# Performance work log

Hardware: AMD Instinct MI355X
Metric: run time of the kernel (lower is better)

Reference implementation:

```python
import jax, jax.numpy as jnp
import numpy as np

D_MODEL = 1024
D_INNER = 2048
D_STATE = 16
D_CONV = 4
DT_RANK = 64  # ceil(D_MODEL / 16)
BATCH = 2
SEQLEN = 2048


def setup_inputs() -> dict:
    key = jax.random.key(0)
    ks = jax.random.split(key, 9)
    s = 0.02
    hidden_states = jax.random.normal(ks[0], (BATCH, SEQLEN, D_MODEL), dtype=jnp.float32)
    W_in = jax.random.normal(ks[1], (D_MODEL, 2 * D_INNER), dtype=jnp.float32) * s
    # flax depthwise Conv kernel layout: (window, in_features//groups=1, out_features)
    conv_kernel = jax.random.normal(ks[2], (D_CONV, 1, D_INNER), dtype=jnp.float32) * 0.2
    conv_bias = jax.random.normal(ks[3], (D_INNER,), dtype=jnp.float32) * s
    W_x = jax.random.normal(ks[4], (D_INNER, DT_RANK + 2 * D_STATE), dtype=jnp.float32) * s
    W_dt = jax.random.normal(ks[5], (DT_RANK, D_INNER), dtype=jnp.float32) * s
    b_dt = jax.random.normal(ks[6], (D_INNER,), dtype=jnp.float32) * s
    # A_log = log(arange(1, d_state+1)) broadcast over d_inner (constant init in module)
    A_log = jnp.log(jnp.broadcast_to(jnp.arange(1, D_STATE + 1, dtype=jnp.float32), (D_INNER, D_STATE)))
    D = jnp.ones((D_INNER,), dtype=jnp.float32)
    W_out = jax.random.normal(ks[7], (D_INNER, D_MODEL), dtype=jnp.float32) * s
    return {
        "hidden_states": hidden_states,
        "W_in": W_in,
        "conv_kernel": conv_kernel,
        "conv_bias": conv_bias,
        "W_x": W_x,
        "W_dt": W_dt,
        "b_dt": b_dt,
        "A_log": A_log,
        "D": D,
        "W_out": W_out,
    }


def _mamba_forward(hidden_states, W_in, conv_kernel, conv_bias, W_x, W_dt, b_dt, A_log, D, W_out):
    # in_proj, then einops '(d i)' split with i=2 => interleaved channels
    xz = hidden_states @ W_in                       # (b, l, 2*d_inner)
    x = xz[..., 0::2]                               # (b, l, d_inner)
    z = xz[..., 1::2]                               # (b, l, d_inner)

    # depthwise conv1d, padding='SAME' (as in flax nn.Conv)
    x = jax.lax.conv_general_dilated(
        x, conv_kernel, window_strides=(1,), padding="SAME",
        dimension_numbers=("NWC", "WIO", "NWC"),
        feature_group_count=D_INNER,
    ) + conv_bias
    x = jax.nn.silu(x)

    x_dbl = x @ W_x                                 # (b, l, dt_rank + 2*d_state)
    dt = x_dbl[..., :DT_RANK] @ W_dt + b_dt         # (b, l, d_inner)
    Bm = x_dbl[..., DT_RANK:DT_RANK + D_STATE]      # (b, l, n)
    Cm = x_dbl[..., DT_RANK + D_STATE:]             # (b, l, n)

    A = -jnp.exp(A_log.astype(jnp.float32))         # (d_inner, n)
    delta = jax.nn.softplus(dt.astype(jnp.float32)) # (b, l, d_inner)

    deltaA = jnp.exp(jnp.einsum("bld,dn->lbdn", delta, A))          # (l, b, d, n)
    deltaB_u = jnp.einsum("bld,bln,bld->lbdn", delta, Bm, x)        # (l, b, d, n)
    C_l = jnp.transpose(Cm, (1, 0, 2))                               # (l, b, n)

    state0 = jnp.zeros((BATCH, D_INNER, D_STATE), dtype=jnp.float32)

    def step(state, inputs):
        dA, dBu, c = inputs
        state = dA * state + dBu                    # (b, d, n)
        y = jnp.einsum("bdn,bn->bd", state, c)      # (b, d)
        return state, y

    _, y = jax.lax.scan(step, state0, (deltaA, deltaB_u, C_l))
    y = jnp.transpose(y, (1, 0, 2))                 # (b, l, d_inner)

    out = (y + x * D) * jax.nn.silu(z)              # skip via D, gate via silu(z)
    return out @ W_out                              # (b, l, d_model)


def reference(hidden_states, W_in, conv_kernel, conv_bias, W_x, W_dt, b_dt, A_log, D, W_out):
    return _mamba_forward(hidden_states, W_in, conv_kernel, conv_bias, W_x, W_dt, b_dt, A_log, D, W_out)
```

## Files before the change

### kernel.cpp

```cpp
#include <hip/hip_runtime.h>
#include <hip/hip_bf16.h>

typedef unsigned short u16;
typedef __attribute__((ext_vector_type(8))) short short8;
typedef __attribute__((ext_vector_type(4))) short short4v;
typedef __attribute__((ext_vector_type(4))) float f32x4;
typedef __attribute__((ext_vector_type(4))) float float4v;
typedef __attribute__((ext_vector_type(2))) float f32x2;

#define DMODEL 1024
#define DI 2048
#define NST 16
#define RANK 64
#define BB 2
#define LL 2048
#define MM (BB*LL)
#define LC 32
#define NCH (LL/LC)

__device__ __forceinline__ float b2f(u16 v){ union{unsigned u; float f;}x; x.u=(unsigned)v<<16; return x.f; }
__device__ __forceinline__ u16 f2b(float f){
  union{unsigned u; float f;}x; x.f=f;
  unsigned r = x.u + 0x7FFFu + ((x.u>>16)&1u);
  return (u16)(r>>16);
}
__device__ __forceinline__ bool probe_bf(const u16* probe){ return probe[1] != 0; }
__device__ __forceinline__ float ldin(const void* p, size_t i, bool bf){
  return bf ? b2f(((const u16*)p)[i]) : ((const float*)p)[i];
}
__device__ __forceinline__ u16 ldb(const void* p, size_t i, bool bf){
  return bf ? ((const u16*)p)[i] : f2b(((const float*)p)[i]);
}
__device__ __forceinline__ void gl16(const u16* g, char* lds_wave_base){
  __builtin_amdgcn_global_load_lds((const __attribute__((address_space(1))) unsigned*)g,
                                   (__attribute__((address_space(3))) unsigned*)lds_wave_base, 16, 0, 0);
}

template<int EPI>
__global__ __launch_bounds__(512,2) void mgemm256_k(
    const u16* __restrict__ A, const u16* __restrict__ Bt,
    void* __restrict__ O0, void* __restrict__ O1,
    int M, int N, int K, int lda, int ldb, int ldc)
{
  __shared__ char smem[131072];
  const int t = threadIdx.x;
  int bx = blockIdx.x, by = blockIdx.y;
  {
    const int gx = gridDim.x;
    const int nwg = gx*gridDim.y;
    const int lin = by*gx + bx;
    const int swz = (lin & 7)*(nwg>>3) + (lin>>3);
    bx = swz % gx; by = swz / gx;
  }
  const int m0 = by*256, n0 = bx*256;
  const int kbeg = blockIdx.z * K;
  const int wv = t >> 6, ln = t & 63;
  const int wr = wv >> 2, wc = wv & 3;
  const int lr = ln & 15, q = ln >> 4;
  const int NT = K >> 6;

  const int srow = ln >> 3;
  const int koff = ((ln & 7) ^ srow) * 8;
  const u16* AgP[4]; const u16* BgP[4];
#pragma unroll
  for(int c=0;c<4;c++){
    AgP[c] = A + (size_t)(m0 + (c*8+wv)*8 + srow)*lda + kbeg + koff;
    BgP[c] = Bt + (size_t)(n0 + (c*8+wv)*8 + srow)*ldb + kbeg + koff;
  }

  const int ck = ((q ^ (ln & 7)) * 16);
  int aro[8], bro[4];
#pragma unroll
  for(int i=0;i<8;i++) aro[i] = (wr*128 + i*16 + lr)*128 + ck;
#pragma unroll
  for(int j=0;j<4;j++) bro[j] = (wc*64 + j*16 + lr)*128 + ck;

  f32x4 acc[8][4];
#pragma unroll
  for(int i=0;i<8;i++)
#pragma unroll
    for(int j=0;j<4;j++) acc[i][j] = (f32x4){0.f,0.f,0.f,0.f};

  auto stage = [&](int kt, int cur){
    char* ab = smem + cur*65536;
    char* bb = ab + 32768;
#pragma unroll
    for(int c=0;c<4;c++) gl16(AgP[c] + kt*64, ab + (c*8+wv)*1024);
#pragma unroll
    for(int c=0;c<4;c++) gl16(BgP[c] + kt*64, bb + (c*8+wv)*1024);
  };

  stage(0,0);
  stage(1,1);

  for(int kt=0; kt<NT; ++kt){
    const int cur = kt & 1;
    if(kt == NT-1) asm volatile("s_waitcnt vmcnt(0)" ::: "memory");
    else           asm volatile("s_waitcnt vmcnt(8)" ::: "memory");
    __builtin_amdgcn_sched_barrier(0);
    __builtin_amdgcn_s_barrier();
    __builtin_amdgcn_sched_barrier(0);
    const char* ab = smem + cur*65536;
    const char* bb = ab + 32768;
    short8 afr[4], bfr[4];
#pragma unroll
    for(int j=0;j<4;j++) bfr[j] = *(const short8*)(bb + bro[j]);
#pragma unroll
    for(int i=0;i<4;i++) afr[i] = *(const short8*)(ab + aro[i]);
    __builtin_amdgcn_s_setprio(1);
#pragma unroll
    for(int i=0;i<4;i++)
#pragma unroll
      for(int j=0;j<4;j++)
        acc[i][j] = __builtin_amdgcn_mfma_f32_16x16x32_bf16(afr[i], bfr[j], acc[i][j], 0,0,0);
    __builtin_amdgcn_s_setprio(0);
#pragma unroll
    for(int i=0;i<4;i++) afr[i] = *(const short8*)(ab + aro[4+i]);
    __builtin_amdgcn_s_setprio(1);
#pragma unroll
    for(int i=0;i<4;i++)
#pragma unroll
      for(int j=0;j<4;j++)
        acc[4+i][j] = __builtin_amdgcn_mfma_f32_16x16x32_bf16(afr[i], bfr[j], acc[4+i][j], 0,0,0);
    __builtin_amdgcn_s_setprio(0);
#pragma unroll
    for(int j=0;j<4;j++) bfr[j] = *(const short8*)(bb + (bro[j]^64));
#pragma unroll
    for(int i=0;i<4;i++) afr[i] = *(const short8*)(ab + (aro[i]^64));
    __builtin_amdgcn_s_setprio(1);
#pragma unroll
    for(int i=0;i<4;i++)
#pragma unroll
      for(int j=0;j<4;j++)
        acc[i][j] = __builtin_amdgcn_mfma_f32_16x16x32_bf16(afr[i], bfr[j], acc[i][j], 0,0,0);
    __builtin_amdgcn_s_setprio(0);
#pragma unroll
    for(int i=0;i<4;i++) afr[i] = *(const short8*)(ab + (aro[4+i]^64));
    asm volatile("s_waitcnt lgkmcnt(0)" ::: "memory");
    __builtin_amdgcn_sched_barrier(0);
    __builtin_amdgcn_s_barrier();
    __builtin_amdgcn_sched_barrier(0);
    if(kt+2 < NT) stage(kt+2, cur);
    __builtin_amdgcn_sched_barrier(0);
    __builtin_amdgcn_s_setprio(1);
#pragma unroll
    for(int i=0;i<4;i++)
#pragma unroll
      for(int j=0;j<4;j++)
        acc[4+i][j] = __builtin_amdgcn_mfma_f32_16x16x32_bf16(afr[i], bfr[j], acc[4+i][j], 0,0,0);
    __builtin_amdgcn_s_setprio(0);
  }

  if(EPI==4){
    u16* tile = (u16*)smem;
    u16* obase = (n0 < DI) ? (u16*)O0 : (u16*)O1;
    const int cb = n0 & (DI-1);
    for(int h=0;h<2;h++){
      __builtin_amdgcn_s_barrier();
      if(wr == h){
#pragma unroll
        for(int i=0;i<8;i++)
#pragma unroll
          for(int r=0;r<4;r++){
            int trow = i*16 + q*4 + r;
#pragma unroll
            for(int j=0;j<4;j++)
              tile[trow*264 + wc*64 + j*16 + lr] = f2b(acc[i][j][r]);
          }
      }
      asm volatile("s_waitcnt lgkmcnt(0)" ::: "memory");
      __builtin_amdgcn_sched_barrier(0);
      __builtin_amdgcn_s_barrier();
      __builtin_amdgcn_sched_barrier(0);
#pragma unroll
      for(int it=0;it<8;it++){
        int idx = it*512 + t;
        int row = idx >> 5;
        int ch  = (idx & 31) * 8;
        short8 v = *(const short8*)(tile + row*264 + ch);
        *(short8*)(obase + (size_t)(m0 + h*128 + row)*ldc + cb + ch) = v;
      }
    }
    return;
  }
#pragma unroll
  for(int i=0;i<8;i++){
#pragma unroll
    for(int r=0;r<4;r++){
      int row = m0 + wr*128 + i*16 + q*4 + r;
#pragma unroll
      for(int j=0;j<4;j++){
        int col = n0 + wc*64 + j*16 + lr;
        ((float*)O0)[(size_t)blockIdx.z*M*ldc + (size_t)row*ldc + col] = acc[i][j][r];
      }
    }
  }
}

template<int EPI>
__global__ __launch_bounds__(256,2) void mgemm_k(
    const u16* __restrict__ A, const u16* __restrict__ Bt,
    void* __restrict__ O0, void* __restrict__ O1,
    const void* __restrict__ bias, const u16* __restrict__ probe,
    int M, int N, int K, int lda, int ldb, int ldc)
{
  const bool bf = probe_bf(probe);
  __shared__ char smem[(EPI==3) ? 33792 : 16384];
  const int t = threadIdx.x;
  int bx = blockIdx.x, by = blockIdx.y;
  {
    const int gx = gridDim.x;
    const int nwg = gx*gridDim.y;
    const int lin = by*gx + bx;
    const int swz = (lin & 7)*(nwg>>3) + (lin>>3);
    bx = swz % gx; by = swz / gx;
  }
  const int m0 = by*128, n0 = bx*128;
  const int kbeg = blockIdx.z * K;
  const int lane = t & 63;
  const int wv = t >> 6;
  const int wm = (wv>>1)*64, wn = (wv&1)*64;
  const int lr = lane & 15, q = lane >> 4;

  const int r0 = t>>2, q0 = t&3;
  const u16* Ag0 = A + kbeg + (size_t)(m0 + r0)*lda + q0*8;
  const u16* Ag1 = A + kbeg + (size_t)(m0 + 64 + r0)*lda + q0*8;
  const u16* Bg0 = Bt + kbeg + (size_t)(n0 + r0)*ldb + q0*8;
  const u16* Bg1 = Bt + kbeg + (size_t)(n0 + 64 + r0)*ldb + q0*8;
  char* const wbase = smem + (t & ~63)*16;
  char* const lA0 = wbase;
  char* const lA1 = wbase + 4096;
  char* const lB0 = wbase + 8192;
  char* const lB1 = wbase + 12288;

  int aro[4], bro[4];
#pragma unroll
  for(int i=0;i<4;i++) aro[i] = (wm + i*16 + lr)*64 + q*16;
#pragma unroll
  for(int j=0;j<4;j++) bro[j] = (wn + j*16 + lr)*64 + q*16;

  f32x4 acc[4][4];
#pragma unroll
  for(int i=0;i<4;i++)
#pragma unroll
    for(int j=0;j<4;j++) acc[i][j] = (f32x4){0.f,0.f,0.f,0.f};

  for(int k0=0;k0<K;k0+=32){
    __syncthreads();
    gl16(Ag0 + k0, lA0); gl16(Ag1 + k0, lA1);
    gl16(Bg0 + k0, lB0); gl16(Bg1 + k0, lB1);
    __syncthreads();
    short8 af[4], bfv[4];
#pragma unroll
    for(int i=0;i<4;i++) af[i] = *(const short8*)(smem + aro[i]);
#pragma unroll
    for(int j=0;j<4;j++) bfv[j] = *(const short8*)(smem + 8192 + bro[j]);
#pragma unroll
    for(int i=0;i<4;i++)
#pragma unroll
      for(int j=0;j<4;j++)
        acc[i][j] = __builtin_amdgcn_mfma_f32_16x16x32_bf16(af[i], bfv[j], acc[i][j], 0,0,0);
  }

  if(EPI==3){
    float bj[4];
#pragma unroll
    for(int j=0;j<4;j++) bj[j] = ldin(bias, n0 + wn + j*16 + lr, bf);
    __syncthreads();
    u16* tile = (u16*)smem;
#pragma unroll
    for(int i=0;i<4;i++)
#pragma unroll
      for(int r=0;r<4;r++){
        int trow = wm + i*16 + q*4 + r;
#pragma unroll
        for(int j=0;j<4;j++){
          int tcol = wn + j*16 + lr;
          float s = acc[i][j][r] + bj[j];
          float sp = (s > 20.f) ? s : log1pf(__expf(s));
          tile[trow*132 + tcol] = f2b(sp);
        }
      }
    __syncthreads();
#pragma unroll
    for(int it=0;it<8;it++){
      int idx = it*256 + t;
      int row = idx >> 4;
      int colc = (idx & 15) * 8;
      short8 v = *(const short8*)(tile + row*132 + colc);
      *(short8*)((u16*)O0 + (size_t)(m0+row)*ldc + n0 + colc) = v;
    }
    return;
  }
#pragma unroll
  for(int i=0;i<4;i++){
#pragma unroll
    for(int r=0;r<4;r++){
      int row = m0 + wm + i*16 + q*4 + r;
#pragma unroll
      for(int j=0;j<4;j++){
        int col = n0 + wn + j*16 + lr;
        ((float*)O0)[(size_t)blockIdx.z*M*ldc + (size_t)row*ldc + col] = acc[i][j][r];
      }
    }
  }
}

__device__ __forceinline__ void tr_block(
    const void* src, u16* dst, int R, int C, int bx, int by, bool bf, bool perm,
    int tid, u16 (*tile)[33])
{
  const int c0 = bx*32, r0 = by*32;
  const int tc = tid & 31, tr0 = tid >> 5;
#pragma unroll
  for(int i=0;i<4;i++){
    int r = tr0 + i*8;
    int gc = c0 + tc;
    tile[r][tc] = (gc < C) ? ldb(src, (size_t)(r0+r)*C + gc, bf) : (u16)0;
  }
  __syncthreads();
#pragma unroll
  for(int i=0;i<4;i++){
    int dr = c0 + tr0 + i*8;
    if(perm) dr = (dr>>1) + ((dr&1)<<11);
    int dc = r0 + tc;
    dst[(size_t)dr*R + dc] = tile[tc][tr0 + i*8];
  }
}

__global__ __launch_bounds__(256) void prep_k(
    const void* __restrict__ W_in, const void* __restrict__ W_out,
    const void* __restrict__ W_x, const void* __restrict__ W_dt,
    const void* __restrict__ hidden,
    u16* __restrict__ WinT, u16* __restrict__ WoutT, u16* __restrict__ WxT,
    u16* __restrict__ WdtT, u16* __restrict__ hb, const u16* __restrict__ probe)
{
  const bool bf = probe_bf(probe);
  __shared__ u16 tile[32][33];
  const int bid = blockIdx.x, t = threadIdx.x;
  if(bid < 4096){
    tr_block(W_in, WinT, DMODEL, 2*DI, bid & 127, bid >> 7, bf, true, t, tile);
  } else if(bid < 6144){
    int b2 = bid - 4096; tr_block(W_out, WoutT, DI, DMODEL, b2 & 31, b2 >> 5, bf, false, t, tile);
  } else if(bid < 6400){
    int b2 = bid - 6144; tr_block(W_x, WxT, DI, 96, b2 & 3, b2 >> 2, bf, false, t, tile);
  } else if(bid < 6528){
    int b2 = bid - 6400; tr_block(W_dt, WdtT, RANK, DI, b2 & 63, b2 >> 6, bf, false, t, tile);
  } else {
    size_t i = ((size_t)(bid - 6528)*256 + t)*8;
    if(bf){
      *(short8*)(hb+i) = *(const short8*)((const u16*)hidden + i);
    } else {
      float4v a = *(const float4v*)((const float*)hidden + i);
      float4v b = *(const float4v*)((const float*)hidden + i + 4);
      short8 r;
      r[0]=(short)f2b(a[0]); r[1]=(short)f2b(a[1]); r[2]=(short)f2b(a[2]); r[3]=(short)f2b(a[3]);
      r[4]=(short)f2b(b[0]); r[5]=(short)f2b(b[1]); r[6]=(short)f2b(b[2]); r[7]=(short)f2b(b[3]);
      *(short8*)(hb+i) = r;
    }
  }
}

__global__ __launch_bounds__(256) void redx_k(
    const float* __restrict__ P, float* __restrict__ xdbl, u16* __restrict__ xdblb)
{
  size_t i = ((size_t)blockIdx.x*256 + threadIdx.x)*4;
  float4v s = *(const float4v*)(P + i);
#pragma unroll
  for(int p=1;p<8;p++) s += *(const float4v*)(P + (size_t)p*MM*128 + i);
  *(float4v*)(xdbl + i) = s;
  short4v r; r[0]=(short)f2b(s[0]); r[1]=(short)f2b(s[1]); r[2]=(short)f2b(s[2]); r[3]=(short)f2b(s[3]);
  *(short4v*)(xdblb + i) = r;
}

__global__ __launch_bounds__(256) void red7_k(
    const float* __restrict__ P, void* __restrict__ out, const u16* __restrict__ probe)
{
  const bool bf = probe_bf(probe);
  size_t i = ((size_t)blockIdx.x*256 + threadIdx.x)*4;
  float4v s = *(const float4v*)(P + i);
#pragma unroll
  for(int p=1;p<4;p++) s += *(const float4v*)(P + (size_t)p*MM*DMODEL + i);
  if(bf){
    short4v r; r[0]=(short)f2b(s[0]); r[1]=(short)f2b(s[1]); r[2]=(short)f2b(s[2]); r[3]=(short)f2b(s[3]);
    *(short4v*)((u16*)out + i) = r;
  } else {
    *(float4v*)((float*)out + i) = s;
  }
}

__global__ __launch_bounds__(256) void conv_silu_k(
  const u16* __restrict__ xb, const void* __restrict__ w,
  const void* __restrict__ bias, u16* __restrict__ xcb,
  const u16* __restrict__ probe)
{
  const bool bf = probe_bf(probe);
  const int row = blockIdx.x;
  const int tt = row & (LL-1);
  const int d = threadIdx.x*8;
  float wv[4][8], bv[8];
  if(bf){
    short8 bb = *(const short8*)((const u16*)bias + d);
#pragma unroll
    for(int j=0;j<8;j++) bv[j] = b2f((u16)bb[j]);
#pragma unroll
    for(int k=0;k<4;k++){
      short8 ww = *(const short8*)((const u16*)w + k*DI + d);
#pragma unroll
      for(int j=0;j<8;j++) wv[k][j] = b2f((u16)ww[j]);
    }
  } else {
    *(float4v*)(bv)   = *(const float4v*)((const float*)bias + d);
    *(float4v*)(bv+4) = *(const float4v*)((const float*)bias + d + 4);
#pragma unroll
    for(int k=0;k<4;k++){
      *(float4v*)(wv[k])   = *(const float4v*)((const float*)w + k*DI + d);
      *(float4v*)(wv[k]+4) = *(const float4v*)((const float*)w + k*DI + d + 4);
    }
  }
  float acc[8];
#pragma unroll
  for(int j=0;j<8;j++) acc[j] = bv[j];
  const u16* xrow = xb + (size_t)row*DI + d;
#pragma unroll
  for(int k=0;k<4;k++){
    int o = tt - 1 + k;
    if(0<=o && o<LL){
      short8 xv = *(const short8*)(xrow + (ptrdiff_t)(k-1)*DI);
#pragma unroll
      for(int j=0;j<8;j++) acc[j] = fmaf(b2f((u16)xv[j]), wv[k][j], acc[j]);
    }
  }
  short8 sb;
#pragma unroll
  for(int j=0;j<8;j++){ float s = acc[j] / (1.f + __expf(-acc[j])); sb[j]=(short)f2b(s); }
  *(short8*)(xcb + (size_t)row*DI + d) = sb;
}

__global__ __launch_bounds__(256) void scan_a_k(
  const u16* __restrict__ dlb, const u16* __restrict__ xcb,
  const float* __restrict__ xdbl, const void* __restrict__ A_log,
  float* __restrict__ Bacc, float* __restrict__ sumdv,
  const u16* __restrict__ probe)
{
  const bool bf = probe_bf(probe);
  __shared__ float Bsh[LC][NST];
  const int t = threadIdx.x;
  const int d0 = blockIdx.x*512 + 2*t;
  const int b = blockIdx.y, c = blockIdx.z;
  for(int i=t;i<LC*NST;i+=256){
    int l = i>>4, n = i&15;
    Bsh[l][n] = xdbl[((size_t)b*LL + (size_t)c*LC + l)*128 + 64 + n];
  }
  __syncthreads();
  float ac[2][NST], s[2][NST];
#pragma unroll
  for(int ch=0;ch<2;ch++)
#pragma unroll
    for(int n=0;n<NST;n++){
      ac[ch][n] = -__expf(ldin(A_log, (size_t)(d0+ch)*NST+n, bf));
      s[ch][n]=0.f;
    }
  bool geom = true;
#pragma unroll
  for(int ch=0;ch<2;ch++){
    float a0 = ac[ch][0];
#pragma unroll
    for(int n=1;n<NST;n++) geom = geom && (fabsf(ac[ch][n]-(n+1)*a0) <= 1e-4f*(n+1)*fabsf(a0));
  }
  float sum0=0.f, sum1=0.f;
  const size_t base0 = ((size_t)b*LL + (size_t)c*LC)*DI + d0;
  const u16* dptr = dlb + base0;
  const u16* xptr = xcb + base0;

  auto stepA = [&](int l, unsigned dp, unsigned xp){
    float dv0=b2f((u16)(dp&0xffff)), dv1=b2f((u16)(dp>>16));
    float xv0=b2f((u16)(xp&0xffff)), xv1=b2f((u16)(xp>>16));
    float du0=dv0*xv0, du1=dv1*xv1;
    sum0+=dv0; sum1+=dv1;
    if(geom){
      float e0=__expf(ac[0][0]*dv0), e1=__expf(ac[1][0]*dv1);
      float p0=1.f, p1=1.f;
#pragma unroll
      for(int n=0;n<NST;n++){
        float Bv=Bsh[l][n];
        p0*=e0; s[0][n]=fmaf(p0, s[0][n], du0*Bv);
        p1*=e1; s[1][n]=fmaf(p1, s[1][n], du1*Bv);
      }
    } else {
#pragma unroll
      for(int n=0;n<NST;n++){
        float Bv=Bsh[l][n];
        s[0][n]=fmaf(__expf(ac[0][n]*dv0), s[0][n], du0*Bv);
        s[1][n]=fmaf(__expf(ac[1][n]*dv1), s[1][n], du1*Bv);
      }
    }
  };

  unsigned dpA = *(const unsigned*)(dptr);
  unsigned xpA = *(const unsigned*)(xptr);
  unsigned dpB = *(const unsigned*)(dptr + DI);
  unsigned xpB = *(const unsigned*)(xptr + DI);
  for(int l=0;l<LC;l+=2){
    int l2 = (l+2 < LC) ? l+2 : LC-1;
    int l3 = (l+3 < LC) ? l+3 : LC-1;
    unsigned dpC = *(const unsigned*)(dptr + (size_t)l2*DI);
    unsigned xpC = *(const unsigned*)(xptr + (size_t)l2*DI);
    unsigned dpD = *(const unsigned*)(dptr + (size_t)l3*DI);
    unsigned xpD = *(const unsigned*)(xptr + (size_t)l3*DI);
    stepA(l,   dpA, xpA);
    stepA(l+1, dpB, xpB);
    dpA=dpC; xpA=xpC; dpB=dpD; xpB=xpD;
  }

  const size_t ob = ((size_t)c*BB + b)*((size_t)NST*DI) + d0;
#pragma unroll
  for(int n=0;n<NST;n++){
    f32x2 bs; bs[0]=s[0][n]; bs[1]=s[1][n];
    *(f32x2*)(Bacc + ob + (size_t)n*DI) = bs;
  }
  f32x2 sd; sd[0]=sum0; sd[1]=sum1;
  *(f32x2*)(sumdv + ((size_t)c*BB + b)*DI + d0) = sd;
}

__global__ __launch_bounds__(256) void scan_b_k(
  const float* __restrict__ Bacc, const float* __restrict__ sumdv,
  const void* __restrict__ A_log, float* __restrict__ Sin,
  const u16* __restrict__ probe)
{
  const bool bf = probe_bf(probe);
  const int idx = blockIdx.x*256 + threadIdx.x;
  const int d = idx & (DI-1);
  const int n = (idx >> 11) & 15;
  const int b = idx >> 15;
  const float ac = -__expf(ldin(A_log, (size_t)d*NST+n, bf));
  float s = 0.f;
  float svN = sumdv[((size_t)0*BB + b)*DI + d];
  float bbN = Bacc[idx];
  for(int c=0;c<NCH;c++){
    int c1 = (c+1 < NCH) ? c+1 : NCH-1;
    float svC = sumdv[((size_t)c1*BB + b)*DI + d];
    float bbC = Bacc[(size_t)c1*((size_t)BB*NST*DI) + idx];
    float a = __expf(ac * svN);
    Sin[(size_t)c*((size_t)BB*NST*DI) + idx] = s;
    s = fmaf(a, s, bbN);
    svN = svC; bbN = bbC;
  }
}

__global__ __launch_bounds__(256) void scan_c_gate_k(
  const u16* __restrict__ dlb, const u16* __restrict__ xcb,
  const float* __restrict__ xdbl, const void* __restrict__ A_log,
  const float* __restrict__ Sin, const u16* __restrict__ zb,
  const void* __restrict__ Dw, u16* __restrict__ G,
  const u16* __restrict__ probe)
{
  const bool bf = probe_bf(probe);
  __shared__ float Bsh[LC][NST], Csh[LC][NST];
  const int t = threadIdx.x;
  const int d0 = blockIdx.x*512 + 2*t;
  const int b = blockIdx.y, c = blockIdx.z;
  for(int i=t;i<LC*NST;i+=256){
    int l = i>>4, n = i&15;
    size_t ro = ((size_t)b*LL + (size_t)c*LC + l)*128;
    Bsh[l][n] = xdbl[ro + 64 + n];
    Csh[l][n] = xdbl[ro + 80 + n];
  }
  __syncthreads();
  float ac[2][NST], s[2][NST];
  const size_t ib = ((size_t)c*BB + b)*((size_t)NST*DI) + d0;
#pragma unroll
  for(int ch=0;ch<2;ch++)
#pragma unroll
    for(int n=0;n<NST;n++)
      ac[ch][n] = -__expf(ldin(A_log, (size_t)(d0+ch)*NST+n, bf));
#pragma unroll
  for(int n=0;n<NST;n++){
    f32x2 si = *(const f32x2*)(Sin + ib + (size_t)n*DI);
    s[0][n]=si[0]; s[1][n]=si[1];
  }
  bool geom = true;
#pragma unroll
  for(int ch=0;ch<2;ch++){
    float a0 = ac[ch][0];
#pragma unroll
    for(int n=1;n<NST;n++) geom = geom && (fabsf(ac[ch][n]-(n+1)*a0) <= 1e-4f*(n+1)*fabsf(a0));
  }
  const float D0 = ldin(Dw, d0, bf), D1 = ldin(Dw, d0+1, bf);
  const size_t base0 = ((size_t)b*LL + (size_t)c*LC)*DI + d0;
  const u16* dptr = dlb + base0;
  const u16* xptr = xcb + base0;
  const u16* zptr = zb  + base0;

  auto stepC = [&](int l, unsigned dp, unsigned xp, unsigned zz){
    float dv0=b2f((u16)(dp&0xffff)), dv1=b2f((u16)(dp>>16));
    float xv0=b2f((u16)(xp&0xffff)), xv1=b2f((u16)(xp>>16));
    float du0=dv0*xv0, du1=dv1*xv1;
    float y0=0.f, y1=0.f;
    if(geom){
      float e0=__expf(ac[0][0]*dv0), e1=__expf(ac[1][0]*dv1);
      float p0=1.f, p1=1.f;
#pragma unroll
      for(int n=0;n<NST;n++){
        float Bv=Bsh[l][n], Cv=Csh[l][n];
        p0*=e0; s[0][n]=fmaf(p0, s[0][n], du0*Bv); y0=fmaf(s[0][n], Cv, y0);
        p1*=e1; s[1][n]=fmaf(p1, s[1][n], du1*Bv); y1=fmaf(s[1][n], Cv, y1);
      }
    } else {
#pragma unroll
      for(int n=0;n<NST;n++){
        float Bv=Bsh[l][n], Cv=Csh[l][n];
        s[0][n]=fmaf(__expf(ac[0][n]*dv0), s[0][n], du0*Bv); y0=fmaf(s[0][n], Cv, y0);
        s[1][n]=fmaf(__expf(ac[1][n]*dv1), s[1][n], du1*Bv); y1=fmaf(s[1][n], Cv, y1);
      }
    }
    float z0 = b2f((u16)(zz & 0xffff)), z1 = b2f((u16)(zz >> 16));
    float g0 = z0 / (1.f + __expf(-z0));
    float g1 = z1 / (1.f + __expf(-z1));
    float o0 = (y0 + xv0*D0) * g0;
    float o1 = (y1 + xv1*D1) * g1;
    *(unsigned*)(G + base0 + (size_t)l*DI) = (unsigned)f2b(o0) | ((unsigned)f2b(o1) << 16);
  };

  unsigned dpA = *(const unsigned*)(dptr);
  unsigned xpA = *(const unsigned*)(xptr);
  unsigned zzA = *(const unsigned*)(zptr);
  unsigned dpB = *(const unsigned*)(dptr + DI);
  unsigned xpB = *(const unsigned*)(xptr + DI);
  unsigned zzB = *(const unsigned*)(zptr + DI);
  for(int l=0;l<LC;l+=2){
    int l2 = (l+2 < LC) ? l+2 : LC-1;
    int l3 = (l+3 < LC) ? l+3 : LC-1;
    unsigned dpC = *(const unsigned*)(dptr + (size_t)l2*DI);
    unsigned xpC = *(const unsigned*)(xptr + (size_t)l2*DI);
    unsigned zzC = *(const unsigned*)(zptr + (size_t)l2*DI);
    unsigned dpD = *(const unsigned*)(dptr + (size_t)l3*DI);
    unsigned xpD = *(const unsigned*)(xptr + (size_t)l3*DI);
    unsigned zzD = *(const unsigned*)(zptr + (size_t)l3*DI);
    stepC(l,   dpA, xpA, zzA);
    stepC(l+1, dpB, xpB, zzB);
    dpA=dpC; xpA=xpC; zzA=zzC; dpB=dpD; xpB=xpD; zzB=zzD;
  }
}

extern "C" void kernel_launch(void* const* d_in, const int* in_sizes, int n_in,
                              void* d_out, int out_size, void* d_ws, size_t ws_size,
                              hipStream_t stream)
{
  const void* hidden = d_in[0];
  const void* W_in   = d_in[1];
  const void* convw  = d_in[2];
  const void* convb  = d_in[3];
  const void* W_x    = d_in[4];
  const void* W_dt   = d_in[5];
  const void* b_dt   = d_in[6];
  const u16*  A_log  = (const u16*)d_in[7];
  const void* Dw     = d_in[8];
  const void* W_out  = d_in[9];

  char* p = (char*)d_ws;
  u16*   xb   = (u16*)  p;
  float* Sin  = (float*)p;
  float* Pw7  = (float*)p;
  u16*   zb   = (u16*)  (p + 16777216);
  u16*   xcb  = (u16*)  (p + 33554432);
  float* Bcc  = (float*)(p + 67108864);
  u16*   G    = (u16*)  (p + 83886080);
  float* Pw   = (float*)(p + 100663296);
  u16*   dlb  = (u16*)  (p + 100663296);
  u16*   hb   = (u16*)  (p + 117440512);
  float* sumdv= (float*)(p + 117440512);
  float* xdbl = (float*)(p + 134217728);
  u16*   xdblb= (u16*)  (p + 136314880);
  u16*   WinT = (u16*)  (p + 137363456);
  u16*   WoutT= (u16*)  (p + 145752064);
  u16*   WxT  = (u16*)  (p + 149946368);
  u16*   WdtT = (u16*)  (p + 150470656);

  prep_k<<<6528 + (MM*DMODEL)/(256*8), 256, 0, stream>>>(
      W_in, W_out, W_x, W_dt, hidden, WinT, WoutT, WxT, WdtT, hb, A_log);
  mgemm256_k<4><<<dim3(16,16), 512, 0, stream>>>(hb, WinT, xb, zb,
                                                 MM, 2*DI, DMODEL, DMODEL, DMODEL, DI);
  conv_silu_k<<<MM, 256, 0, stream>>>(xb, convw, convb, xcb, A_log);
  mgemm_k<1><<<dim3(1,32,8), 256, 0, stream>>>(xcb, WxT, Pw, nullptr, nullptr, A_log,
                                               MM, 128, DI/8, DI, DI, 128);
  redx_k<<<(MM*128)/(256*4), 256, 0, stream>>>(Pw, xdbl, xdblb);
  mgemm_k<3><<<dim3(16,32), 256, 0, stream>>>(xdblb, WdtT, dlb, nullptr, b_dt, A_log,
                                              MM, DI, RANK, 128, RANK, DI);
  scan_a_k<<<dim3(DI/512, BB, NCH), 256, 0, stream>>>(dlb, xcb, xdbl, A_log, Bcc, sumdv, A_log);
  scan_b_k<<<(BB*NST*DI)/256, 256, 0, stream>>>(Bcc, sumdv, A_log, Sin, A_log);
  scan_c_gate_k<<<dim3(DI/512, BB, NCH), 256, 0, stream>>>(dlb, xcb, xdbl, A_log, Sin, zb, Dw, G, A_log);
  mgemm256_k<1><<<dim3(4,16,4), 512, 0, stream>>>(G, WoutT, Pw7, nullptr,
                                                  MM, DMODEL, DI/4, DI, DI, DMODEL);
  red7_k<<<(MM*DMODEL)/(256*4), 256, 0, stream>>>(Pw7, d_out, A_log);
}
```

Measured before the change: 325.3 us.

## Quad-buffer 256x256 GEMM with K=32 stages and split scan to one channel per thread

The 256x256 MFMA GEMM now stages K in 32-wide slices across four LDS buffers with a three-deep prefetch, issuing the A and B loads separately between the two MFMA halves. It uses a new swizzle and waits on vmcnt counts that shrink near the tail. The goal is to overlap global-to-LDS copies with MFMA work more finely, at the cost of more barriers per unit of K. The scan kernels change from two channels per thread to one, which doubles the grid and adds a launch-bounds occupancy hint to raise wave parallelism, while making the global loads and stores 16-bit instead of 32-bit.

Measured after the change: 436.2 us. 34.1% more time.

```diff
diff --git a/kernel.cpp b/kernel.cpp
--- a/kernel.cpp
+++ b/kernel.cpp
@@ -57,23 +57,21 @@
   const int wv = t >> 6, ln = t & 63;
   const int wr = wv >> 2, wc = wv & 3;
   const int lr = ln & 15, q = ln >> 4;
-  const int NT = K >> 6;
-
-  const int srow = ln >> 3;
-  const int koff = ((ln & 7) ^ srow) * 8;
-  const u16* AgP[4]; const u16* BgP[4];
-#pragma unroll
-  for(int c=0;c<4;c++){
-    AgP[c] = A + (size_t)(m0 + (c*8+wv)*8 + srow)*lda + kbeg + koff;
-    BgP[c] = Bt + (size_t)(n0 + (c*8+wv)*8 + srow)*ldb + kbeg + koff;
-  }
-
-  const int ck = ((q ^ (ln & 7)) * 16);
+  const int NT = K >> 5;
+
+  const int srow = ln >> 2;
+  const int koff = (((ln&3) ^ (srow&3)) * 8);
+  const u16* gA0 = A  + (size_t)(m0 +       wv*16 + srow)*lda + kbeg + koff;
+  const u16* gA1 = A  + (size_t)(m0 + 128 + wv*16 + srow)*lda + kbeg + koff;
+  const u16* gB0 = Bt + (size_t)(n0 +       wv*16 + srow)*ldb + kbeg + koff;
+  const u16* gB1 = Bt + (size_t)(n0 + 128 + wv*16 + srow)*ldb + kbeg + koff;
+
+  const int ck = (q ^ (lr & 3)) * 16;
   int aro[8], bro[4];
 #pragma unroll
-  for(int i=0;i<8;i++) aro[i] = (wr*128 + i*16 + lr)*128 + ck;
-#pragma unroll
-  for(int j=0;j<4;j++) bro[j] = (wc*64 + j*16 + lr)*128 + ck;
+  for(int i=0;i<8;i++) aro[i] = (wr*128 + i*16 + lr)*64 + ck;
+#pragma unroll
+  for(int j=0;j<4;j++) bro[j] = 16384 + (wc*64 + j*16 + lr)*64 + ck;
 
   f32x4 acc[8][4];
 #pragma unroll
@@ -81,32 +79,37 @@
 #pragma unroll
     for(int j=0;j<4;j++) acc[i][j] = (f32x4){0.f,0.f,0.f,0.f};
 
-  auto stage = [&](int kt, int cur){
-    char* ab = smem + cur*65536;
-    char* bb = ab + 32768;
-#pragma unroll
-    for(int c=0;c<4;c++) gl16(AgP[c] + kt*64, ab + (c*8+wv)*1024);
-#pragma unroll
-    for(int c=0;c<4;c++) gl16(BgP[c] + kt*64, bb + (c*8+wv)*1024);
+  auto stageA = [&](int kt){
+    char* b = smem + (kt&3)*32768;
+    gl16(gA0 + kt*32, b + wv*1024);
+    gl16(gA1 + kt*32, b + 8192 + wv*1024);
   };
-
-  stage(0,0);
-  stage(1,1);
+  auto stageB = [&](int kt){
+    char* b = smem + (kt&3)*32768 + 16384;
+    gl16(gB0 + kt*32, b + wv*1024);
+    gl16(gB1 + kt*32, b + 8192 + wv*1024);
+  };
+
+  stageA(0); stageB(0);
+  stageA(1); stageB(1);
+  stageA(2); stageB(2);
+  asm volatile("s_waitcnt vmcnt(8)" ::: "memory");
+  __builtin_amdgcn_sched_barrier(0);
+  __builtin_amdgcn_s_barrier();
+  __builtin_amdgcn_sched_barrier(0);
 
   for(int kt=0; kt<NT; ++kt){
-    const int cur = kt & 1;
-    if(kt == NT-1) asm volatile("s_waitcnt vmcnt(0)" ::: "memory");
-    else           asm volatile("s_waitcnt vmcnt(8)" ::: "memory");
+    const char* base = smem + (kt&3)*32768;
+    short8 bfr[4], afr[4];
+#pragma unroll
+    for(int j=0;j<4;j++) bfr[j] = *(const short8*)(base + bro[j]);
+#pragma unroll
+    for(int i=0;i<4;i++) afr[i] = *(const short8*)(base + aro[i]);
+    if(kt+3 < NT) stageA(kt+3);
     __builtin_amdgcn_sched_barrier(0);
     __builtin_amdgcn_s_barrier();
-    __builtin_amdgcn_sched_barrier(0);
-    const char* ab = smem + cur*65536;
-    const char* bb = ab + 32768;
-    short8 afr[4], bfr[4];
-#pragma unroll
-    for(int j=0;j<4;j++) bfr[j] = *(const short8*)(bb + bro[j]);
-#pragma unroll
-    for(int i=0;i<4;i++) afr[i] = *(const short8*)(ab + aro[i]);
+    asm volatile("s_waitcnt lgkmcnt(0)" ::: "memory");
+    __builtin_amdgcn_sched_barrier(0);
     __builtin_amdgcn_s_setprio(1);
 #pragma unroll
     for(int i=0;i<4;i++)
@@ -114,8 +117,19 @@
       for(int j=0;j<4;j++)
         acc[i][j] = __builtin_amdgcn_mfma_f32_16x16x32_bf16(afr[i], bfr[j], acc[i][j], 0,0,0);
     __builtin_amdgcn_s_setprio(0);
-#pragma unroll
-    for(int i=0;i<4;i++) afr[i] = *(const short8*)(ab + aro[4+i]);
+    __builtin_amdgcn_sched_barrier(0);
+    __builtin_amdgcn_s_barrier();
+    __builtin_amdgcn_sched_barrier(0);
+#pragma unroll
+    for(int i=0;i<4;i++) afr[i] = *(const short8*)(base + aro[4+i]);
+    if(kt+3 < NT) stageB(kt+3);
+    if(kt+3 < NT)      asm volatile("s_waitcnt vmcnt(8)" ::: "memory");
+    else if(kt+2 < NT) asm volatile("s_waitcnt vmcnt(4)" ::: "memory");
+    else if(kt+1 < NT) asm volatile("s_waitcnt vmcnt(0)" ::: "memory");
+    __builtin_amdgcn_sched_barrier(0);
+    __builtin_amdgcn_s_barrier();
+    asm volatile("s_waitcnt lgkmcnt(0)" ::: "memory");
+    __builtin_amdgcn_sched_barrier(0);
     __builtin_amdgcn_s_setprio(1);
 #pragma unroll
     for(int i=0;i<4;i++)
@@ -123,32 +137,9 @@
       for(int j=0;j<4;j++)
         acc[4+i][j] = __builtin_amdgcn_mfma_f32_16x16x32_bf16(afr[i], bfr[j], acc[4+i][j], 0,0,0);
     __builtin_amdgcn_s_setprio(0);
-#pragma unroll
-    for(int j=0;j<4;j++) bfr[j] = *(const short8*)(bb + (bro[j]^64));
-#pragma unroll
-    for(int i=0;i<4;i++) afr[i] = *(const short8*)(ab + (aro[i]^64));
-    __builtin_amdgcn_s_setprio(1);
-#pragma unroll
-    for(int i=0;i<4;i++)
-#pragma unroll
-      for(int j=0;j<4;j++)
-        acc[i][j] = __builtin_amdgcn_mfma_f32_16x16x32_bf16(afr[i], bfr[j], acc[i][j], 0,0,0);
-    __builtin_amdgcn_s_setprio(0);
-#pragma unroll
-    for(int i=0;i<4;i++) afr[i] = *(const short8*)(ab + (aro[4+i]^64));
-    asm volatile("s_waitcnt lgkmcnt(0)" ::: "memory");
     __builtin_amdgcn_sched_barrier(0);
     __builtin_amdgcn_s_barrier();
     __builtin_amdgcn_sched_barrier(0);
-    if(kt+2 < NT) stage(kt+2, cur);
-    __builtin_amdgcn_sched_barrier(0);
-    __builtin_amdgcn_s_setprio(1);
-#pragma unroll
-    for(int i=0;i<4;i++)
-#pragma unroll
-      for(int j=0;j<4;j++)
-        acc[4+i][j] = __builtin_amdgcn_mfma_f32_16x16x32_bf16(afr[i], bfr[j], acc[4+i][j], 0,0,0);
-    __builtin_amdgcn_s_setprio(0);
   }
 
   if(EPI==4){
@@ -437,7 +428,7 @@
   *(short8*)(xcb + (size_t)row*DI + d) = sb;
 }
 
-__global__ __launch_bounds__(256) void scan_a_k(
+__global__ __launch_bounds__(256,4) void scan_a_k(
   const u16* __restrict__ dlb, const u16* __restrict__ xcb,
   const float* __restrict__ xdbl, const void* __restrict__ A_log,
   float* __restrict__ Bacc, float* __restrict__ sumdv,
@@ -446,68 +437,55 @@
   const bool bf = probe_bf(probe);
   __shared__ float Bsh[LC][NST];
   const int t = threadIdx.x;
-  const int d0 = blockIdx.x*512 + 2*t;
+  const int d0 = blockIdx.x*256 + t;
   const int b = blockIdx.y, c = blockIdx.z;
   for(int i=t;i<LC*NST;i+=256){
     int l = i>>4, n = i&15;
     Bsh[l][n] = xdbl[((size_t)b*LL + (size_t)c*LC + l)*128 + 64 + n];
   }
   __syncthreads();
-  float ac[2][NST], s[2][NST];
-#pragma unroll
-  for(int ch=0;ch<2;ch++)
-#pragma unroll
-    for(int n=0;n<NST;n++){
-      ac[ch][n] = -__expf(ldin(A_log, (size_t)(d0+ch)*NST+n, bf));
-      s[ch][n]=0.f;
-    }
+  float ac[NST], s[NST];
+#pragma unroll
+  for(int n=0;n<NST;n++){
+    ac[n] = -__expf(ldin(A_log, (size_t)d0*NST+n, bf));
+    s[n]=0.f;
+  }
   bool geom = true;
-#pragma unroll
-  for(int ch=0;ch<2;ch++){
-    float a0 = ac[ch][0];
-#pragma unroll
-    for(int n=1;n<NST;n++) geom = geom && (fabsf(ac[ch][n]-(n+1)*a0) <= 1e-4f*(n+1)*fabsf(a0));
-  }
-  float sum0=0.f, sum1=0.f;
+  {
+    float a0 = ac[0];
+#pragma unroll
+    for(int n=1;n<NST;n++) geom = geom && (fabsf(ac[n]-(n+1)*a0) <= 1e-4f*(n+1)*fabsf(a0));
+  }
+  float sum=0.f;
   const size_t base0 = ((size_t)b*LL + (size_t)c*LC)*DI + d0;
   const u16* dptr = dlb + base0;
   const u16* xptr = xcb + base0;
 
-  auto stepA = [&](int l, unsigned dp, unsigned xp){
-    float dv0=b2f((u16)(dp&0xffff)), dv1=b2f((u16)(dp>>16));
-    float xv0=b2f((u16)(xp&0xffff)), xv1=b2f((u16)(xp>>16));
-    float du0=dv0*xv0, du1=dv1*xv1;
-    sum0+=dv0; sum1+=dv1;
+  auto stepA = [&](int l, u16 dp, u16 xp){
+    float dv=b2f(dp), xv=b2f(xp);
+    float du=dv*xv;
+    sum+=dv;
     if(geom){
-      float e0=__expf(ac[0][0]*dv0), e1=__expf(ac[1][0]*dv1);
-      float p0=1.f, p1=1.f;
+      float e=__expf(ac[0]*dv);
+      float p=1.f;
 #pragma unroll
       for(int n=0;n<NST;n++){
-        float Bv=Bsh[l][n];
-        p0*=e0; s[0][n]=fmaf(p0, s[0][n], du0*Bv);
-        p1*=e1; s[1][n]=fmaf(p1, s[1][n], du1*Bv);
+        p*=e; s[n]=fmaf(p, s[n], du*Bsh[l][n]);
       }
     } else {
 #pragma unroll
-      for(int n=0;n<NST;n++){
-        float Bv=Bsh[l][n];
-        s[0][n]=fmaf(__expf(ac[0][n]*dv0), s[0][n], du0*Bv);
-        s[1][n]=fmaf(__expf(ac[1][n]*dv1), s[1][n], du1*Bv);
-      }
+      for(int n=0;n<NST;n++)
+        s[n]=fmaf(__expf(ac[n]*dv), s[n], du*Bsh[l][n]);
     }
   };
 
-  unsigned dpA = *(const unsigned*)(dptr);
-  unsigned xpA = *(const unsigned*)(xptr);
-  unsigned dpB = *(const unsigned*)(dptr + DI);
-  unsigned xpB = *(const unsigned*)(xptr + DI);
+  u16 dpA = dptr[0], xpA = xptr[0];
+  u16 dpB = dptr[DI], xpB = xptr[DI];
   for(int l=0;l<LC;l+=2){
     int l2 = (l+2 < LC) ? l+2 : LC-1;
     int l3 = (l+3 < LC) ? l+3 : LC-1;
-    unsigned dpC = *(const unsigned*)(dptr + (size_t)l2*DI);
-    unsigned xpC = *(const unsigned*)(xptr + (size_t)l2*DI);
-    unsigned dpD = *(const unsigned*)(dptr + (size_t)l3*DI);
-    unsigned xpD = *(const unsigned*)(xptr + (size_t)l3*DI);
+    u16 dpC = dptr[(size_t)l2*DI], xpC = xptr[(size_t)l2*DI];
+    u16 dpD = dptr[(size_t)l3*DI], xpD = xptr[(size_t)l3*DI];
     stepA(l,   dpA, xpA);
     stepA(l+1, dpB, xpB);
     dpA=dpC; xpA=xpC; dpB=dpD; xpB=xpD;
@@ -515,12 +493,8 @@
 
   const size_t ob = ((size_t)c*BB + b)*((size_t)NST*DI) + d0;
 #pragma unroll
-  for(int n=0;n<NST;n++){
-    f32x2 bs; bs[0]=s[0][n]; bs[1]=s[1][n];
-    *(f32x2*)(Bacc + ob + (size_t)n*DI) = bs;
-  }
-  f32x2 sd; sd[0]=sum0; sd[1]=sum1;
-  *(f32x2*)(sumdv + ((size_t)c*BB + b)*DI + d0) = sd;
+  for(int n=0;n<NST;n++) Bacc[ob + (size_t)n*DI] = s[n];
+  sumdv[((size_t)c*BB + b)*DI + d0] = sum;
 }
 
 __global__ __launch_bounds__(256) void scan_b_k(
@@ -548,7 +522,7 @@
   }
 }
 
-__global__ __launch_bounds__(256) void scan_c_gate_k(
+__global__ __launch_bounds__(256,4) void scan_c_gate_k(
   const u16* __restrict__ dlb, const u16* __restrict__ xcb,
   const float* __restrict__ xdbl, const void* __restrict__ A_log,
   const float* __restrict__ Sin, const u16* __restrict__ zb,
@@ -558,7 +532,7 @@
   const bool bf = probe_bf(probe);
   __shared__ float Bsh[LC][NST], Csh[LC][NST];
   const int t = threadIdx.x;
-  const int d0 = blockIdx.x*512 + 2*t;
+  const int d0 = blockIdx.x*256 + t;
   const int b = blockIdx.y, c = blockIdx.z;
   for(int i=t;i<LC*NST;i+=256){
     int l = i>>4, n = i&15;
@@ -567,76 +541,55 @@
     Csh[l][n] = xdbl[ro + 80 + n];
   }
   __syncthreads();
-  float ac[2][NST], s[2][NST];
+  float ac[NST], s[NST];
   const size_t ib = ((size_t)c*BB + b)*((size_t)NST*DI) + d0;
 #pragma unroll
-  for(int ch=0;ch<2;ch++)
-#pragma unroll
-    for(int n=0;n<NST;n++)
-      ac[ch][n] = -__expf(ldin(A_log, (size_t)(d0+ch)*NST+n, bf));
-#pragma unroll
-  for(int n=0;n<NST;n++){
-    f32x2 si = *(const f32x2*)(Sin + ib + (size_t)n*DI);
-    s[0][n]=si[0]; s[1][n]=si[1];
-  }
+  for(int n=0;n<NST;n++)
+    ac[n] = -__expf(ldin(A_log, (size_t)d0*NST+n, bf));
+#pragma unroll
+  for(int n=0;n<NST;n++) s[n] = Sin[ib + (size_t)n*DI];
   bool geom = true;
-#pragma unroll
-  for(int ch=0;ch<2;ch++){
-    float a0 = ac[ch][0];
-#pragma unroll
-    for(int n=1;n<NST;n++) geom = geom && (fabsf(ac[ch][n]-(n+1)*a0) <= 1e-4f*(n+1)*fabsf(a0));
-  }
-  const float D0 = ldin(Dw, d0, bf), D1 = ldin(Dw, d0+1, bf);
+  {
+    float a0 = ac[0];
+#pragma unroll
+    for(int n=1;n<NST;n++) geom = geom && (fabsf(ac[n]-(n+1)*a0) <= 1e-4f*(n+1)*fabsf(a0));
+  }
+  const float D0 = ldin(Dw, d0, bf);
   const size_t base0 = ((size_t)b*LL + (size_t)c*LC)*DI + d0;
   const u16* dptr = dlb + base0;
   const u16* xptr = xcb + base0;
   const u16* zptr = zb  + base0;
 
-  auto stepC = [&](int l, unsigned dp, unsigned xp, unsigned zz){
-    float dv0=b2f((u16)(dp&0xffff)), dv1=b2f((u16)(dp>>16));
-    float xv0=b2f((u16)(xp&0xffff)), xv1=b2f((u16)(xp>>16));
-    float du0=dv0*xv0, du1=dv1*xv1;
-    float y0=0.f, y1=0.f;
+  auto stepC = [&](int l, u16 dp, u16 xp, u16 zz){
+    float dv=b2f(dp), xv=b2f(xp);
+    float du=dv*xv;
+    float y=0.f;
     if(geom){
-      float e0=__expf(ac[0][0]*dv0), e1=__expf(ac[1][0]*dv1);
-      float p0=1.f, p1=1.f;
+      float e=__expf(ac[0]*dv);
+      float p=1.f;
 #pragma unroll
       for(int n=0;n<NST;n++){
-        float Bv=Bsh[l][n], Cv=Csh[l][n];
-        p0*=e0; s[0][n]=fmaf(p0, s[0][n], du0*Bv); y0=fmaf(s[0][n], Cv, y0);
-        p1*=e1; s[1][n]=fmaf(p1, s[1][n], du1*Bv); y1=fmaf(s[1][n], Cv, y1);
+        p*=e; s[n]=fmaf(p, s[n], du*Bsh[l][n]); y=fmaf(s[n], Csh[l][n], y);
       }
     } else {
 #pragma unroll
       for(int n=0;n<NST;n++){
-        float Bv=Bsh[l][n], Cv=Csh[l][n];
-        s[0][n]=fmaf(__expf(ac[0][n]*dv0), s[0][n], du0*Bv); y0=fmaf(s[0][n], Cv, y0);
-        s[1][n]=fmaf(__expf(ac[1][n]*dv1), s[1][n], du1*Bv); y1=fmaf(s[1][n], Cv, y1);
-      }
-    }
-    float z0 = b2f((u16)(zz & 0xffff)), z1 = b2f((u16)(zz >> 16));
+        s[n]=fmaf(__expf(ac[n]*dv), s[n], du*Bsh[l][n]); y=fmaf(s[n], Csh[l][n], y);
+      }
+    }
+    float z0 = b2f(zz);
     float g0 = z0 / (1.f + __expf(-z0));
-    float g1 = z1 / (1.f + __expf(-z1));
-    float o0 = (y0 + xv0*D0) * g0;
-    float o1 = (y1 + xv1*D1) * g1;
-    *(unsigned*)(G + base0 + (size_t)l*DI) = (unsigned)f2b(o0) | ((unsigned)f2b(o1) << 16);
+    float o0 = (y + xv*D0) * g0;
+    G[base0 + (size_t)l*DI] = f2b(o0);
   };
 
-  unsigned dpA = *(const unsigned*)(dptr);
-  unsigned xpA = *(const unsigned*)(xptr);
-  unsigned zzA = *(const unsigned*)(zptr);
-  unsigned dpB = *(const unsigned*)(dptr + DI);
-  unsigned xpB = *(const unsigned*)(xptr + DI);
-  unsigned zzB = *(const unsigned*)(zptr + DI);
+  u16 dpA = dptr[0], xpA = xptr[0], zzA = zptr[0];
+  u16 dpB = dptr[DI], xpB = xptr[DI], zzB = zptr[DI];
   for(int l=0;l<LC;l+=2){
     int l2 = (l+2 < LC) ? l+2 : LC-1;
     int l3 = (l+3 < LC) ? l+3 : LC-1;
-    unsigned dpC = *(const unsigned*)(dptr + (size_t)l2*DI);
-    unsigned xpC = *(const unsigned*)(xptr + (size_t)l2*DI);
-    unsigned zzC = *(const unsigned*)(zptr + (size_t)l2*DI);
-    unsigned dpD = *(const unsigned*)(dptr + (size_t)l3*DI);
-    unsigned xpD = *(const unsigned*)(xptr + (size_t)l3*DI);
-    unsigned zzD = *(const unsigned*)(zptr + (size_t)l3*DI);
+    u16 dpC = dptr[(size_t)l2*DI], xpC = xptr[(size_t)l2*DI], zzC = zptr[(size_t)l2*DI];
+    u16 dpD = dptr[(size_t)l3*DI], xpD = xptr[(size_t)l3*DI], zzD = zptr[(size_t)l3*DI];
     stepC(l,   dpA, xpA, zzA);
     stepC(l+1, dpB, xpB, zzB);
     dpA=dpC; xpA=xpC; zzA=zzC; dpB=dpD; xpB=xpD; zzB=zzD;
@@ -687,9 +640,9 @@
   redx_k<<<(MM*128)/(256*4), 256, 0, stream>>>(Pw, xdbl, xdblb);
   mgemm_k<3><<<dim3(16,32), 256, 0, stream>>>(xdblb, WdtT, dlb, nullptr, b_dt, A_log,
                                               MM, DI, RANK, 128, RANK, DI);
-  scan_a_k<<<dim3(DI/512, BB, NCH), 256, 0, stream>>>(dlb, xcb, xdbl, A_log, Bcc, sumdv, A_log);
+  scan_a_k<<<dim3(DI/256, BB, NCH), 256, 0, stream>>>(dlb, xcb, xdbl, A_log, Bcc, sumdv, A_log);
   scan_b_k<<<(BB*NST*DI)/256, 256, 0, stream>>>(Bcc, sumdv, A_log, Sin, A_log);
-  scan_c_gate_k<<<dim3(DI/512, BB, NCH), 256, 0, stream>>>(dlb, xcb, xdbl, A_log, Sin, zb, Dw, G, A_log);
+  scan_c_gate_k<<<dim3(DI/256, BB, NCH), 256, 0, stream>>>(dlb, xcb, xdbl, A_log, Sin, zb, Dw, G, A_log);
   mgemm256_k<1><<<dim3(4,16,4), 512, 0, stream>>>(G, WoutT, Pw7, nullptr,
                                                   MM, DMODEL, DI/4, DI, DI, DMODEL);
   red7_k<<<(MM*DMODEL)/(256*4), 256, 0, stream>>>(Pw7, d_out, A_log);
```
